# Optimization experiments

Measured on AMD Instinct MI355X. Metric: run time of the kernel, lower is better.

Reference implementation:

```python
import jax, jax.numpy as jnp
import numpy as np

N = 50000       # nodes
E = 1250000     # edges
DIM = 64
H = 16
DPH = DIM // H  # 4
LN_EPS = 1e-5


def setup_inputs() -> dict:
    key = jax.random.key(0)
    ks = jax.random.split(key, 10)
    return {
        "node_feat": jax.random.normal(ks[0], (N, DIM), jnp.float32),
        "edge_feat": jax.random.normal(ks[1], (E, H, DPH), jnp.float32),
        "node_vec": jax.random.normal(ks[2], (N, 3, DIM), jnp.float32),
        "radial": jax.random.uniform(ks[3], (E,), jnp.float32),
        "ln_g": jnp.ones((DIM,), jnp.float32),
        "ln_b": jnp.zeros((DIM,), jnp.float32),
        "qkv_w": jax.random.normal(ks[4], (DIM, 3 * DIM), jnp.float32) / np.sqrt(DIM).astype(np.float32),
        "qkv_b": jnp.zeros((3 * DIM,), jnp.float32),
        "vec_w": jax.random.normal(ks[5], (DIM, 2 * DIM), jnp.float32) / np.sqrt(DIM).astype(np.float32),
        "out_w": jax.random.normal(ks[6], (DIM, 2 * DIM), jnp.float32) / np.sqrt(DIM).astype(np.float32),
        "out_b": jnp.zeros((2 * DIM,), jnp.float32),
        "row": jax.random.randint(ks[7], (E,), 0, N, jnp.int32),
        "col": jax.random.randint(ks[8], (E,), 0, N, jnp.int32),
        "natoms": N,
    }


def reference(node_feat, edge_feat, node_vec, radial, ln_g, ln_b,
              qkv_w, qkv_b, vec_w, out_w, out_b, row, col, natoms):
    # LayerNorm (biased variance, as torch)
    mu = jnp.mean(node_feat, axis=-1, keepdims=True)
    var = jnp.mean(jnp.square(node_feat - mu), axis=-1, keepdims=True)
    x = (node_feat - mu) * jax.lax.rsqrt(var + LN_EPS) * ln_g + ln_b

    # QKV projection -> [N, H, 3*DPH], split
    qkv = (x @ qkv_w + qkv_b).reshape(-1, H, 3 * DPH)
    q = qkv[..., :DPH]
    k = qkv[..., DPH:2 * DPH]
    v = qkv[..., 2 * DPH:]

    # Gather by edge indices, gated dot-product attention per edge  [E, H]
    attn = jax.nn.gelu(jnp.sum(q[row] * k[col], axis=-1), approximate=False) * radial[:, None]

    # Equivariant vector gate  [N, DIM]
    iv = node_vec @ vec_w  # [N, 3, 2*DIM]
    input_dot = jnp.sum(iv[..., :DIM] * iv[..., DIM:], axis=-2)

    # Edge messages and scatter-add into nodes
    m = v[col] * edge_feat * attn[..., None]          # [E, H, DPH]
    m_agg = jax.ops.segment_sum(m, row, num_segments=natoms)  # [N, H, DPH]
    m_agg = m_agg.reshape(natoms, DIM)

    out = m_agg @ out_w + out_b                        # [N, 2*DIM]
    return input_dot * out[..., :DIM] + out[..., DIM:]
```

## Files before the change

### kernel.cpp

```cpp
#include <hip/hip_runtime.h>
#include <math.h>

#define DIM 64
#define NW 4
#define NPB 4
#define CAP 64
#define PIPE 4

__device__ __forceinline__ float waveReduceSum(float v) {
    #pragma unroll
    for (int off = 1; off < 64; off <<= 1)
        v += __shfl_xor(v, off, 64);
    return v;
}

__global__ __launch_bounds__(256) void qkv_kernel(
    const float* __restrict__ node_feat,
    const float* __restrict__ ln_g, const float* __restrict__ ln_b,
    const float* __restrict__ qkv_w, const float* __restrict__ qkv_b,
    float* __restrict__ q, float* __restrict__ k, float* __restrict__ v,
    int N)
{
    __shared__ float  wlds[64 * 192];
    __shared__ float4 xs[NW][NPB][16];
    const int wave = threadIdx.x >> 6, lane = threadIdx.x & 63;

    for (int idx = threadIdx.x; idx < 64 * 192; idx += 256) {
        int d = idx / 192, j = idx - d * 192;
        int jj = j & 63, sec = j >> 6;
        int c = 12 * (jj >> 2) + (jj & 3) + 4 * sec;
        wlds[idx] = qkv_w[d * 192 + c];
    }
    const int c0 = 12 * (lane >> 2) + (lane & 3);
    const float b0 = qkv_b[c0], b1 = qkv_b[c0 + 4], b2 = qkv_b[c0 + 8];
    const float gg = ln_g[lane], bb = ln_b[lane];
    __syncthreads();

    const int nstride = gridDim.x * NW * NPB;
    for (int n0 = (blockIdx.x * NW + wave) * NPB; n0 < N; n0 += nstride) {
        const int cnt = min(NPB, N - n0);
        float acc0[NPB], acc1[NPB], acc2[NPB];
        #pragma unroll
        for (int i = 0; i < NPB; ++i) {
            acc0[i] = b0; acc1[i] = b1; acc2[i] = b2;
            if (i < cnt) {
                float nf = node_feat[(size_t)(n0 + i) * DIM + lane];
                float mu = waveReduceSum(nf) * (1.0f / 64.0f);
                float dv = nf - mu;
                float var = waveReduceSum(dv * dv) * (1.0f / 64.0f);
                float x = dv * rsqrtf(var + 1e-5f) * gg + bb;
                ((float*)&xs[wave][i][0])[lane] = x;
            }
        }
        #pragma unroll 4
        for (int d4 = 0; d4 < 16; ++d4) {
            float4 xv[NPB];
            #pragma unroll
            for (int i = 0; i < NPB; ++i) xv[i] = xs[wave][i][d4];
            #pragma unroll
            for (int u = 0; u < 4; ++u) {
                int d = d4 * 4 + u;
                float w0 = wlds[d * 192 + lane];
                float w1 = wlds[d * 192 + lane + 64];
                float w2 = wlds[d * 192 + lane + 128];
                #pragma unroll
                for (int i = 0; i < NPB; ++i) {
                    float xd = (&xv[i].x)[u];
                    acc0[i] = fmaf(xd, w0, acc0[i]);
                    acc1[i] = fmaf(xd, w1, acc1[i]);
                    acc2[i] = fmaf(xd, w2, acc2[i]);
                }
            }
        }
        #pragma unroll
        for (int i = 0; i < NPB; ++i) if (i < cnt) {
            size_t off = (size_t)(n0 + i) * DIM + lane;
            q[off] = acc0[i]; k[off] = acc1[i]; v[off] = acc2[i];
        }
    }
}

__global__ __launch_bounds__(256) void vec_kernel(
    const float* __restrict__ node_vec,
    const float* __restrict__ vec_w,
    float* __restrict__ input_dot,
    const int* __restrict__ row,
    const int* __restrict__ col,
    int* __restrict__ deg,
    int2* __restrict__ perm2,
    int* __restrict__ ovcnt,
    int* __restrict__ ovlist,
    int N, int E)
{
    __shared__ float  vlds[64 * 128];
    __shared__ float4 nvs[NW][NPB][3][16];
    const int wave = threadIdx.x >> 6, lane = threadIdx.x & 63;

    for (int idx = threadIdx.x; idx < 64 * 128; idx += 256)
        vlds[idx] = vec_w[idx];
    __syncthreads();

    const int nstride = gridDim.x * NW * NPB;
    for (int n0 = (blockIdx.x * NW + wave) * NPB; n0 < N; n0 += nstride) {
        const int cnt = min(NPB, N - n0);
        float a0[NPB][3], a1[NPB][3];
        #pragma unroll
        for (int i = 0; i < NPB; ++i) {
            #pragma unroll
            for (int s = 0; s < 3; ++s) {
                a0[i][s] = 0.f; a1[i][s] = 0.f;
                if (i < cnt)
                    ((float*)&nvs[wave][i][s][0])[lane] =
                        node_vec[((size_t)(n0 + i) * 3 + s) * DIM + lane];
            }
        }
        #pragma unroll 2
        for (int d4 = 0; d4 < 16; ++d4) {
            #pragma unroll
            for (int u = 0; u < 4; ++u) {
                int d = d4 * 4 + u;
                float w0 = vlds[d * 128 + lane];
                float w1 = vlds[d * 128 + lane + 64];
                #pragma unroll
                for (int i = 0; i < NPB; ++i) {
                    #pragma unroll
                    for (int s = 0; s < 3; ++s) {
                        float nv = ((float*)&nvs[wave][i][s][d4])[u];
                        a0[i][s] = fmaf(nv, w0, a0[i][s]);
                        a1[i][s] = fmaf(nv, w1, a1[i][s]);
                    }
                }
            }
        }
        #pragma unroll
        for (int i = 0; i < NPB; ++i) if (i < cnt) {
            size_t off = (size_t)(n0 + i) * DIM + lane;
            input_dot[off] = a0[i][0] * a1[i][0] + a0[i][1] * a1[i][1]
                           + a0[i][2] * a1[i][2];
        }
    }

    for (int e = blockIdx.x * 256 + threadIdx.x; e < E; e += gridDim.x * 256) {
        int r = row[e];
        int slot = atomicAdd(&deg[r], 1);
        if (slot < CAP) {
            perm2[(size_t)r * CAP + slot] = make_int2(e, col[e]);
        } else {
            int o = atomicAdd(ovcnt, 1);
            ovlist[o] = e;
        }
    }
}

__global__ __launch_bounds__(256) void ovf_kernel(
    const float* __restrict__ q,
    const float* __restrict__ k,
    const float* __restrict__ v,
    const float* __restrict__ edge_feat,
    const float* __restrict__ radial,
    const int* __restrict__ row,
    const int* __restrict__ col,
    const int* __restrict__ ovcnt,
    const int* __restrict__ ovlist,
    float* __restrict__ m_agg)
{
    const int wave = threadIdx.x >> 6, lane = threadIdx.x & 63;
    const int ovn = *ovcnt;
    for (int i = blockIdx.x * NW + wave; i < ovn; i += gridDim.x * NW) {
        int e = ovlist[i];
        int r = row[e], c = col[e];
        float p = q[(size_t)r * DIM + lane] * k[(size_t)c * DIM + lane];
        p += __shfl_xor(p, 1, 64);
        p += __shfl_xor(p, 2, 64);
        float g = 0.5f * p * (1.0f + erff(p * 0.70710678118654752f));
        float a = g * radial[e];
        float m = v[(size_t)c * DIM + lane] * edge_feat[(size_t)e * DIM + lane] * a;
        atomicAdd(&m_agg[(size_t)r * DIM + lane], m);
    }
}

__global__ __launch_bounds__(256) void agg_kernel(
    const float* __restrict__ q,
    const float* __restrict__ kptr,
    const float* __restrict__ vptr,
    const float* __restrict__ edge_feat,
    const float* __restrict__ radial,
    const int2* __restrict__ perm2,
    const int* __restrict__ deg,
    const float* __restrict__ m_agg,
    const float* __restrict__ input_dot,
    const float* __restrict__ out_w,
    const float* __restrict__ out_b,
    float* __restrict__ result,
    int N)
{
    __shared__ float accs[NW][64];
    const int wave = threadIdx.x >> 6, lane = threadIdx.x & 63;
    const float ob0 = out_b[lane], ob1 = out_b[lane + 64];

#define ISSUE(J, S) do {                                                   \
        if ((J) < cn) {                                                    \
            int e_ = __shfl(myec.x, (J), 64);                              \
            int c_ = __shfl(myec.y, (J), 64);                              \
            kq[S] = kptr[(c_ << 6) + lane];                                \
            vq[S] = vptr[(c_ << 6) + lane];                                \
            eq[S] = __builtin_nontemporal_load(                            \
                        &edge_feat[((size_t)(unsigned)e_ << 6) + lane]);   \
        }                                                                  \
    } while (0)

    for (int n = blockIdx.x * NW + wave; n < N; n += gridDim.x * NW) {
        const int draw = deg[n];
        const int cn = min(draw, CAP);
        int2 myec = make_int2(0, 0);
        float myrad = 0.0f;
        if (lane < cn) {
            myec = perm2[(size_t)n * CAP + lane];
            myrad = radial[myec.x];
        }
        const float qd = q[(n << 6) + lane];
        float idv = input_dot[(n << 6) + lane];

        float kq[PIPE], vq[PIPE], eq[PIPE];
        #pragma unroll
        for (int s = 0; s < PIPE; ++s) ISSUE(s, s);

        float acc = 0.0f;
        for (int j0 = 0; j0 < cn; j0 += PIPE) {
            #pragma unroll
            for (int s = 0; s < PIPE; ++s) {
                const int j = j0 + s;
                if (j < cn) {
                    float kd = kq[s], vd = vq[s], ef = eq[s];
                    ISSUE(j + PIPE, s);
                    float rad = __shfl(myrad, j, 64);
                    float p = qd * kd;
                    p += __shfl_xor(p, 1, 64);
                    p += __shfl_xor(p, 2, 64);
                    float g = 0.5f * p *
                              (1.0f + erff(p * 0.70710678118654752f));
                    acc = fmaf(vd * ef, g * rad, acc);
                }
            }
        }

        if (draw > CAP) acc += m_agg[(n << 6) + lane];

        accs[wave][lane] = acc;
        float o0 = ob0, o1 = ob1;
        #pragma unroll 8
        for (int d = 0; d < 64; ++d) {
            float md = accs[wave][d];
            o0 = fmaf(md, out_w[d * 128 + lane], o0);
            o1 = fmaf(md, out_w[d * 128 + 64 + lane], o1);
        }
        result[(n << 6) + lane] = idv * o0 + o1;
    }
#undef ISSUE
}

extern "C" void kernel_launch(void* const* d_in, const int* in_sizes, int n_in,
                              void* d_out, int out_size, void* d_ws, size_t ws_size,
                              hipStream_t stream)
{
    const float* node_feat = (const float*)d_in[0];
    const float* edge_feat = (const float*)d_in[1];
    const float* node_vec  = (const float*)d_in[2];
    const float* radial    = (const float*)d_in[3];
    const float* ln_g      = (const float*)d_in[4];
    const float* ln_b      = (const float*)d_in[5];
    const float* qkv_w     = (const float*)d_in[6];
    const float* qkv_b     = (const float*)d_in[7];
    const float* vec_w     = (const float*)d_in[8];
    const float* out_w     = (const float*)d_in[9];
    const float* out_b     = (const float*)d_in[10];
    const int*   row       = (const int*)d_in[11];
    const int*   col       = (const int*)d_in[12];

    const int N = in_sizes[0] / DIM;
    const int E = in_sizes[3];

    float* ws    = (float*)d_ws;
    float* q     = ws;
    float* k     = q    + (size_t)N * DIM;
    float* v     = k    + (size_t)N * DIM;
    float* idot  = v    + (size_t)N * DIM;
    float* m_agg = idot + (size_t)N * DIM;
    int2*  perm2 = (int2*)(m_agg + (size_t)N * DIM);
    int*   deg   = (int*)(perm2 + (size_t)N * CAP);
    int*   ovcnt = deg + N;
    int*   ovlist= ovcnt + 1;

    const int grid_nodes = 768;
    const int grid_agg   = (N + NW - 1) / NW;

    hipMemsetAsync(m_agg, 0, (size_t)N * DIM * sizeof(float), stream);
    hipMemsetAsync(deg,   0, (size_t)(N + 1) * sizeof(int), stream);

    qkv_kernel<<<grid_nodes, 256, 0, stream>>>(node_feat, ln_g, ln_b,
                                               qkv_w, qkv_b, q, k, v, N);
    vec_kernel<<<grid_nodes, 256, 0, stream>>>(node_vec, vec_w, idot,
                                               row, col, deg, perm2,
                                               ovcnt, ovlist, N, E);
    ovf_kernel<<<256, 256, 0, stream>>>(q, k, v, edge_feat, radial,
                                        row, col, ovcnt, ovlist, m_agg);
    agg_kernel<<<grid_agg, 256, 0, stream>>>(q, k, v, edge_feat, radial,
                                             perm2, deg, m_agg, idot,
                                             out_w, out_b, (float*)d_out, N);
}
```

Before: 762.5 us.

## Interleave K and V into float2 buffer and batch GELU across lanes

Result: slower. 783.1 us (+2.7%).

```diff
diff --git a/kernel.cpp b/kernel.cpp
--- a/kernel.cpp
+++ b/kernel.cpp
@@ -18,7 +18,7 @@
     const float* __restrict__ node_feat,
     const float* __restrict__ ln_g, const float* __restrict__ ln_b,
     const float* __restrict__ qkv_w, const float* __restrict__ qkv_b,
-    float* __restrict__ q, float* __restrict__ k, float* __restrict__ v,
+    float* __restrict__ q, float2* __restrict__ kv,
     int N)
 {
     __shared__ float  wlds[64 * 192];
@@ -75,7 +75,8 @@
         #pragma unroll
         for (int i = 0; i < NPB; ++i) if (i < cnt) {
             size_t off = (size_t)(n0 + i) * DIM + lane;
-            q[off] = acc0[i]; k[off] = acc1[i]; v[off] = acc2[i];
+            q[off] = acc0[i];
+            kv[off] = make_float2(acc1[i], acc2[i]);
         }
     }
 }
@@ -154,8 +155,7 @@
 
 __global__ __launch_bounds__(256) void ovf_kernel(
     const float* __restrict__ q,
-    const float* __restrict__ k,
-    const float* __restrict__ v,
+    const float2* __restrict__ kv,
     const float* __restrict__ edge_feat,
     const float* __restrict__ radial,
     const int* __restrict__ row,
@@ -169,20 +169,20 @@
     for (int i = blockIdx.x * NW + wave; i < ovn; i += gridDim.x * NW) {
         int e = ovlist[i];
         int r = row[e], c = col[e];
-        float p = q[(size_t)r * DIM + lane] * k[(size_t)c * DIM + lane];
+        float2 kvv = kv[(size_t)c * DIM + lane];
+        float p = q[(size_t)r * DIM + lane] * kvv.x;
         p += __shfl_xor(p, 1, 64);
         p += __shfl_xor(p, 2, 64);
         float g = 0.5f * p * (1.0f + erff(p * 0.70710678118654752f));
         float a = g * radial[e];
-        float m = v[(size_t)c * DIM + lane] * edge_feat[(size_t)e * DIM + lane] * a;
+        float m = kvv.y * edge_feat[(size_t)e * DIM + lane] * a;
         atomicAdd(&m_agg[(size_t)r * DIM + lane], m);
     }
 }
 
 __global__ __launch_bounds__(256) void agg_kernel(
     const float* __restrict__ q,
-    const float* __restrict__ kptr,
-    const float* __restrict__ vptr,
+    const float2* __restrict__ kv,
     const float* __restrict__ edge_feat,
     const float* __restrict__ radial,
     const int2* __restrict__ perm2,
@@ -196,14 +196,14 @@
 {
     __shared__ float accs[NW][64];
     const int wave = threadIdx.x >> 6, lane = threadIdx.x & 63;
+    const int l3 = lane & 3, lh = lane & 60;
     const float ob0 = out_b[lane], ob1 = out_b[lane + 64];
 
 #define ISSUE(J, S) do {                                                   \
         if ((J) < cn) {                                                    \
             int e_ = __shfl(myec.x, (J), 64);                              \
             int c_ = __shfl(myec.y, (J), 64);                              \
-            kq[S] = kptr[(c_ << 6) + lane];                                \
-            vq[S] = vptr[(c_ << 6) + lane];                                \
+            kvq[S] = kv[(c_ << 6) + lane];                                 \
             eq[S] = __builtin_nontemporal_load(                            \
                         &edge_feat[((size_t)(unsigned)e_ << 6) + lane]);   \
         }                                                                  \
@@ -221,26 +221,37 @@
         const float qd = q[(n << 6) + lane];
         float idv = input_dot[(n << 6) + lane];
 
-        float kq[PIPE], vq[PIPE], eq[PIPE];
+        float2 kvq[PIPE]; float eq[PIPE];
         #pragma unroll
         for (int s = 0; s < PIPE; ++s) ISSUE(s, s);
 
         float acc = 0.0f;
         for (int j0 = 0; j0 < cn; j0 += PIPE) {
+            float p[PIPE], ve[PIPE], rad[PIPE];
             #pragma unroll
             for (int s = 0; s < PIPE; ++s) {
                 const int j = j0 + s;
                 if (j < cn) {
-                    float kd = kq[s], vd = vq[s], ef = eq[s];
+                    float kd = kvq[s].x, vd = kvq[s].y, ef = eq[s];
                     ISSUE(j + PIPE, s);
-                    float rad = __shfl(myrad, j, 64);
-                    float p = qd * kd;
-                    p += __shfl_xor(p, 1, 64);
-                    p += __shfl_xor(p, 2, 64);
-                    float g = 0.5f * p *
-                              (1.0f + erff(p * 0.70710678118654752f));
-                    acc = fmaf(vd * ef, g * rad, acc);
-                }
+                    ve[s] = vd * ef;
+                    rad[s] = __shfl(myrad, j, 64);
+                    float pp = qd * kd;
+                    pp += __shfl_xor(pp, 1, 64);
+                    pp += __shfl_xor(pp, 2, 64);
+                    p[s] = pp;
+                } else { p[s] = 0.f; ve[s] = 0.f; rad[s] = 0.f; }
+            }
+            float psel = l3 == 0 ? p[0] : l3 == 1 ? p[1]
+                       : l3 == 2 ? p[2] : p[3];
+            float rsel = l3 == 0 ? rad[0] : l3 == 1 ? rad[1]
+                       : l3 == 2 ? rad[2] : rad[3];
+            float aval = 0.5f * psel *
+                         (1.0f + erff(psel * 0.70710678118654752f)) * rsel;
+            #pragma unroll
+            for (int s = 0; s < PIPE; ++s) {
+                if (j0 + s < cn)
+                    acc = fmaf(ve[s], __shfl(aval, lh + s, 64), acc);
             }
         }
 
@@ -280,16 +291,15 @@
     const int N = in_sizes[0] / DIM;
     const int E = in_sizes[3];
 
-    float* ws    = (float*)d_ws;
-    float* q     = ws;
-    float* k     = q    + (size_t)N * DIM;
-    float* v     = k    + (size_t)N * DIM;
-    float* idot  = v    + (size_t)N * DIM;
-    float* m_agg = idot + (size_t)N * DIM;
-    int2*  perm2 = (int2*)(m_agg + (size_t)N * DIM);
-    int*   deg   = (int*)(perm2 + (size_t)N * CAP);
-    int*   ovcnt = deg + N;
-    int*   ovlist= ovcnt + 1;
+    float*  ws    = (float*)d_ws;
+    float*  q     = ws;
+    float2* kv    = (float2*)(q + (size_t)N * DIM);
+    float*  idot  = (float*)(kv + (size_t)N * DIM);
+    float*  m_agg = idot + (size_t)N * DIM;
+    int2*   perm2 = (int2*)(m_agg + (size_t)N * DIM);
+    int*    deg   = (int*)(perm2 + (size_t)N * CAP);
+    int*    ovcnt = deg + N;
+    int*    ovlist= ovcnt + 1;
 
     const int grid_nodes = 768;
     const int grid_agg   = (N + NW - 1) / NW;
@@ -298,13 +308,13 @@
     hipMemsetAsync(deg,   0, (size_t)(N + 1) * sizeof(int), stream);
 
     qkv_kernel<<<grid_nodes, 256, 0, stream>>>(node_feat, ln_g, ln_b,
-                                               qkv_w, qkv_b, q, k, v, N);
+                                               qkv_w, qkv_b, q, kv, N);
     vec_kernel<<<grid_nodes, 256, 0, stream>>>(node_vec, vec_w, idot,
                                                row, col, deg, perm2,
                                                ovcnt, ovlist, N, E);
-    ovf_kernel<<<256, 256, 0, stream>>>(q, k, v, edge_feat, radial,
+    ovf_kernel<<<256, 256, 0, stream>>>(q, kv, edge_feat, radial,
                                         row, col, ovcnt, ovlist, m_agg);
-    agg_kernel<<<grid_agg, 256, 0, stream>>>(q, k, v, edge_feat, radial,
+    agg_kernel<<<grid_agg, 256, 0, stream>>>(q, kv, edge_feat, radial,
                                              perm2, deg, m_agg, idot,
                                              out_w, out_b, (float*)d_out, N);
 }
```
